# Performance work log

Hardware: AMD Instinct MI355X
Metric: run time of the kernel (lower is better)

## Reference

```python
import jax, jax.numpy as jnp
import numpy as np


def setup_inputs() -> dict:
    key = jax.random.key(0)
    k1, k2, k3 = jax.random.split(key, 3)
    B, H, N, D = 4, 16, 4096, 128
    return {
        "q": jax.random.normal(k1, (B, H, N, D), dtype=jnp.float32),
        "k": jax.random.normal(k2, (B, H, N, D), dtype=jnp.float32),
        "v": jax.random.normal(k3, (B, H, N, D), dtype=jnp.float32),
    }


def reference(q, k, v):
    # Aaren-style numerically stable online-softmax linear-attention scan.
    # q, k, v: [B, H, N, D]
    scale = 1.0
    B, H, N, D = q.shape
    qs = jnp.moveaxis(q * scale, 2, 0)  # [N, B, H, D] time-major
    ks = jnp.moveaxis(k, 2, 0)
    vs = jnp.moveaxis(v, 2, 0)

    n0 = jnp.zeros((B, H, D), dtype=q.dtype)
    d0 = jnp.zeros((B, H, 1), dtype=q.dtype)
    m0 = jnp.full((B, H, 1), -jnp.inf, dtype=q.dtype)

    def step(carry, inp):
        n_p, d_p, m_p = carry
        q_t, k_t, v_t = inp
        alpha = jnp.sum(q_t * k_t, axis=-1, keepdims=True)  # [B, H, 1]
        m_t = jnp.maximum(m_p, alpha)
        exp_mdiff = jnp.exp(m_p - m_t)
        exp_adiff = jnp.exp(alpha - m_t)
        d_t = exp_mdiff * d_p + exp_adiff
        n_t = exp_mdiff * n_p + exp_adiff * v_t
        y_t = n_t / d_t
        return (n_t, d_t, m_t), y_t

    _, y = jax.lax.scan(step, (n0, d0, m0), (qs, ks, vs))  # y: [N, B, H, D]
    return jnp.moveaxis(y, 0, 2)  # [B, H, N, D]
```

## Files before the change

kernel.cpp:

```cpp
#include <hip/hip_runtime.h>
#include <math.h>
#include <stdint.h>

static constexpr int ROWS = 64;
static constexpr int NSEQ = 4096;
static constexpr int DIM  = 128;
static constexpr int SC   = 16;
static constexpr int SPR  = NSEQ / SC;
static constexpr int NSC  = ROWS * SPR;
static constexpr int VC   = 64;
static constexpr int VPR  = NSEQ / VC;
static constexpr int NVC  = ROWS * VPR;
static constexpr int SPC  = VC / SC;

__global__ __launch_bounds__(256) void k_alpha(
    const float* __restrict__ q, const float* __restrict__ k,
    float* __restrict__ alpha, float* __restrict__ cM, float* __restrict__ cD)
{
    const int lane = threadIdx.x & 31;
    const int g    = blockIdx.x * 8 + (threadIdx.x >> 5);
    const int t    = lane >> 1;
    const int h    = lane & 1;
    const float* qb = q + (size_t)g * (SC * DIM) + t * DIM + h * 64;
    const float* kb = k + (size_t)g * (SC * DIM) + t * DIM + h * 64;

    float acc = 0.f;
    #pragma unroll
    for (int u0 = 0; u0 < 64; u0 += 16) {
        float4 q4[4], k4[4];
        #pragma unroll
        for (int j = 0; j < 4; ++j) q4[j] = *(const float4*)(qb + u0 + j * 4);
        #pragma unroll
        for (int j = 0; j < 4; ++j) k4[j] = *(const float4*)(kb + u0 + j * 4);
        __builtin_amdgcn_sched_barrier(0);
        #pragma unroll
        for (int j = 0; j < 4; ++j)
            acc += q4[j].x * k4[j].x + q4[j].y * k4[j].y
                 + q4[j].z * k4[j].z + q4[j].w * k4[j].w;
    }
    acc += __shfl_xor(acc, 1);

    float M = acc;
    M = fmaxf(M, __shfl_xor(M, 2));
    M = fmaxf(M, __shfl_xor(M, 4));
    M = fmaxf(M, __shfl_xor(M, 8));
    M = fmaxf(M, __shfl_xor(M, 16));
    float e = (h == 0) ? __expf(acc - M) : 0.f;
    e += __shfl_xor(e, 2);
    e += __shfl_xor(e, 4);
    e += __shfl_xor(e, 8);
    e += __shfl_xor(e, 16);

    if (h == 0) alpha[g * SC + t] = acc;
    if (lane == 0) { cM[g] = M; cD[g] = e; }
}

__global__ __launch_bounds__(256) void k_scan(
    const float* __restrict__ alpha, const float* __restrict__ cM,
    const float* __restrict__ cD,
    float* __restrict__ pM, float* __restrict__ pD, float2* __restrict__ coefCW)
{
    __shared__ float lM[SPR], lD[SPR], lpM[SPR];
    const int row = blockIdx.x;
    const int tid = threadIdx.x;

    lM[tid] = cM[row * SPR + tid];
    lD[tid] = cD[row * SPR + tid];
    __syncthreads();

    if (tid == 0) {
        float m = -INFINITY, d = 0.f;
        for (int sl = 0; sl < SPR; ++sl) {
            lpM[sl] = m;
            pM[row * SPR + sl] = m; pD[row * SPR + sl] = d;
            const float M = lM[sl], D = lD[sl];
            const float mn = fmaxf(m, M);
            d = d * __expf(m - mn) + D * __expf(M - mn);
            m = mn;
        }
    }
    __syncthreads();

    const int li = tid & 15, grp = tid >> 4;
    for (int sl = grp; sl < SPR; sl += 16) {
        const int s = row * SPR + sl;
        const float a = alpha[s * SC + li];
        float m = a;
        #pragma unroll
        for (int d = 1; d < 16; d <<= 1) {
            const float o = __shfl_up(m, d, 16);
            if (li >= d) m = fmaxf(m, o);
        }
        const float carry = lpM[sl];
        const float mf = fmaxf(m, carry);
        float mp = __shfl_up(mf, 1, 16);
        if (li == 0) mp = carry;
        const float cc = __expf(mp - mf);
        const float wt = __expf(a - mf);
        coefCW[s * SC + li] = make_float2(cc, wt);
    }
}

__global__ __launch_bounds__(256) void k_agg(
    const float* __restrict__ v, const float2* __restrict__ coefCW,
    float2* __restrict__ aggN)
{
    const int lane  = threadIdx.x & 63;
    const int C     = blockIdx.x * 4 + (threadIdx.x >> 6);
    const int vbase = C * (VC * DIM);
    const int cbase = __builtin_amdgcn_readfirstlane(C * VC);

    float nx = 0.f, ny = 0.f;
    for (int t0 = 0; t0 < VC; t0 += 8) {
        float2 cw[8], vv[8];
        #pragma unroll
        for (int u = 0; u < 8; ++u) cw[u] = coefCW[cbase + t0 + u];
        #pragma unroll
        for (int u = 0; u < 8; ++u)
            vv[u] = *((const float2*)(v + vbase + (t0 + u) * DIM) + lane);
        #pragma unroll
        for (int u = 0; u < 8; ++u) {
            nx = cw[u].x * nx + cw[u].y * vv[u].x;
            ny = cw[u].x * ny + cw[u].y * vv[u].y;
        }
    }
    aggN[C * (DIM / 2) + lane] = make_float2(nx, ny);
}

__global__ __launch_bounds__(128) void k_pref(
    float* __restrict__ aggN, const float* __restrict__ pM)
{
    const int row = blockIdx.x;
    const int d   = threadIdx.x;
    float state = 0.f;
    for (int C0 = 0; C0 < VPR; C0 += 8) {
        float nb[8], f1[8];
        #pragma unroll
        for (int u = 0; u < 8; ++u) {
            const int C  = C0 + u;
            const int Cg = row * VPR + C;
            nb[u] = aggN[Cg * DIM + d];
            const bool last = (C == VPR - 1);
            const float mp  = pM[SPC * Cg];
            const float mp2 = last ? 0.f : pM[SPC * Cg + SPC];
            f1[u] = last ? 0.f : __expf(mp - mp2);
        }
        #pragma unroll
        for (int u = 0; u < 8; ++u) {
            const float nc = nb[u];
            aggN[(row * VPR + C0 + u) * DIM + d] = state;
            state = state * f1[u] + nc;
        }
    }
}

__global__ __launch_bounds__(256) void k_out(
    const float* __restrict__ v, const float2* __restrict__ coefCW,
    const float2* __restrict__ preN, const float* __restrict__ pD,
    float* __restrict__ y)
{
    const int lane  = threadIdx.x & 63;
    const int C     = blockIdx.x * 4 + (threadIdx.x >> 6);
    const int vbase = C * (VC * DIM);
    const int cbase = __builtin_amdgcn_readfirstlane(C * VC);

    float2 n  = preN[C * (DIM / 2) + lane];
    float dch = pD[SPC * C];

    for (int t0 = 0; t0 < VC; t0 += 8) {
        float2 cw[8], vv[8];
        #pragma unroll
        for (int u = 0; u < 8; ++u) cw[u] = coefCW[cbase + t0 + u];
        #pragma unroll
        for (int u = 0; u < 8; ++u)
            vv[u] = *((const float2*)(v + vbase + (t0 + u) * DIM) + lane);
        #pragma unroll
        for (int u = 0; u < 8; ++u) {
            n.x = cw[u].x * n.x + cw[u].y * vv[u].x;
            n.y = cw[u].x * n.y + cw[u].y * vv[u].y;
            dch = cw[u].x * dch + cw[u].y;
            const float rd = __builtin_amdgcn_rcpf(dch);
            *((float2*)(y + vbase + (t0 + u) * DIM) + lane) =
                make_float2(n.x * rd, n.y * rd);
        }
    }
}

extern "C" void kernel_launch(void* const* d_in, const int* in_sizes, int n_in,
                              void* d_out, int out_size, void* d_ws, size_t ws_size,
                              hipStream_t stream) {
    const float* q = (const float*)d_in[0];
    const float* k = (const float*)d_in[1];
    const float* v = (const float*)d_in[2];
    float* y  = (float*)d_out;
    float* ws = (float*)d_ws;

    float*  coefCWf = ws;
    float*  pM      = coefCWf + 2 * ROWS * NSEQ;
    float*  pD      = pM + NSC;
    float*  cM      = pD + NSC;
    float*  cD      = cM + NSC;
    float*  U       = cD + NSC;
    float*  alphaA  = U;
    float*  aggNf   = U;
    float2* coefCW  = (float2*)coefCWf;
    float2* aggN2   = (float2*)aggNf;

    k_alpha<<<NSC / 8, 256, 0, stream>>>(q, k, alphaA, cM, cD);
    k_scan<<<ROWS, 256, 0, stream>>>(alphaA, cM, cD, pM, pD, coefCW);
    k_agg<<<NVC / 4, 256, 0, stream>>>(v, coefCW, aggN2);
    k_pref<<<ROWS, DIM, 0, stream>>>(aggNf, pM);
    k_out<<<NVC / 4, 256, 0, stream>>>(v, coefCW, aggN2, pD, y);
}
```

Measured before the change: 175.8 us.

## Stage q/k tiles into LDS via direct global-to-LDS loads in k_alpha

Rewrites the alpha kernel so each 256-thread block handles one 16-row chunk. It loads q and k straight into shared memory with global_load_lds using an XOR swizzle, then reads swizzled float4s to compute partial dot products and reduces them across waves through shared memory. The aim is fully coalesced, asynchronous loads and more blocks in flight in place of per-thread strided float4 loads. In exchange it adds two block barriers and much more LDS per block, and only 16 threads do the final reduction.

Result: faster. 159.6 us (-9.2%).

```diff
diff --git a/kernel.cpp b/kernel.cpp
--- a/kernel.cpp
+++ b/kernel.cpp
@@ -13,46 +13,69 @@
 static constexpr int NVC  = ROWS * VPR;
 static constexpr int SPC  = VC / SC;
 
+typedef __attribute__((address_space(3))) uint32_t  lds_u32;
+typedef const __attribute__((address_space(1))) uint32_t g_u32;
+
 __global__ __launch_bounds__(256) void k_alpha(
     const float* __restrict__ q, const float* __restrict__ k,
     float* __restrict__ alpha, float* __restrict__ cM, float* __restrict__ cD)
 {
-    const int lane = threadIdx.x & 31;
-    const int g    = blockIdx.x * 8 + (threadIdx.x >> 5);
-    const int t    = lane >> 1;
-    const int h    = lane & 1;
-    const float* qb = q + (size_t)g * (SC * DIM) + t * DIM + h * 64;
-    const float* kb = k + (size_t)g * (SC * DIM) + t * DIM + h * 64;
-
-    float acc = 0.f;
+    __shared__ float qs[2048];
+    __shared__ float ks[2048];
+    __shared__ float aw[4][16];
+    const int tid = threadIdx.x;
+    const int l   = tid & 63;
+    const int w   = tid >> 6;
+    const int s   = blockIdx.x;
+    const size_t base = (size_t)s * (SC * DIM);
+
     #pragma unroll
-    for (int u0 = 0; u0 < 64; u0 += 16) {
-        float4 q4[4], k4[4];
-        #pragma unroll
-        for (int j = 0; j < 4; ++j) q4[j] = *(const float4*)(qb + u0 + j * 4);
-        #pragma unroll
-        for (int j = 0; j < 4; ++j) k4[j] = *(const float4*)(kb + u0 + j * 4);
-        __builtin_amdgcn_sched_barrier(0);
-        #pragma unroll
-        for (int j = 0; j < 4; ++j)
-            acc += q4[j].x * k4[j].x + q4[j].y * k4[j].y
-                 + q4[j].z * k4[j].z + q4[j].w * k4[j].w;
-    }
-    acc += __shfl_xor(acc, 1);
-
-    float M = acc;
-    M = fmaxf(M, __shfl_xor(M, 2));
-    M = fmaxf(M, __shfl_xor(M, 4));
-    M = fmaxf(M, __shfl_xor(M, 8));
-    M = fmaxf(M, __shfl_xor(M, 16));
-    float e = (h == 0) ? __expf(acc - M) : 0.f;
-    e += __shfl_xor(e, 2);
-    e += __shfl_xor(e, 4);
-    e += __shfl_xor(e, 8);
-    e += __shfl_xor(e, 16);
-
-    if (h == 0) alpha[g * SC + t] = acc;
-    if (lane == 0) { cM[g] = M; cD[g] = e; }
+    for (int r = 0; r < 2; ++r) {
+        const int p  = r * 4096 + tid * 16;
+        const int ps = p ^ (((p >> 9) & 7) << 4);
+        __builtin_amdgcn_global_load_lds((g_u32*)(q + base + (ps >> 2)),
+            (lds_u32*)&qs[(r * 4096 + w * 1024) >> 2], 16, 0, 0);
+    }
+    #pragma unroll
+    for (int r = 0; r < 2; ++r) {
+        const int p  = r * 4096 + tid * 16;
+        const int ps = p ^ (((p >> 9) & 7) << 4);
+        __builtin_amdgcn_global_load_lds((g_u32*)(k + base + (ps >> 2)),
+            (lds_u32*)&ks[(r * 4096 + w * 1024) >> 2], 16, 0, 0);
+    }
+    __syncthreads();
+
+    const int row = l & 15;
+    const int cb  = (l >> 4) + 4 * w;
+    const int swz = (row & 7) << 4;
+    float part = 0.f;
+    #pragma unroll
+    for (int rr = 0; rr < 2; ++rr) {
+        const int off = row * 512 + ((cb * 32 + rr * 16) ^ swz);
+        const float4 qv = *(const float4*)((const char*)qs + off);
+        const float4 kv = *(const float4*)((const char*)ks + off);
+        part += qv.x * kv.x + qv.y * kv.y + qv.z * kv.z + qv.w * kv.w;
+    }
+    part += __shfl_xor(part, 16);
+    part += __shfl_xor(part, 32);
+    if (l < 16) aw[w][row] = part;
+    __syncthreads();
+
+    if (tid < 16) {
+        const float a = aw[0][tid] + aw[1][tid] + aw[2][tid] + aw[3][tid];
+        float M = a;
+        M = fmaxf(M, __shfl_xor(M, 1));
+        M = fmaxf(M, __shfl_xor(M, 2));
+        M = fmaxf(M, __shfl_xor(M, 4));
+        M = fmaxf(M, __shfl_xor(M, 8));
+        float e = __expf(a - M);
+        e += __shfl_xor(e, 1);
+        e += __shfl_xor(e, 2);
+        e += __shfl_xor(e, 4);
+        e += __shfl_xor(e, 8);
+        alpha[s * SC + tid] = a;
+        if (tid == 0) { cM[s] = M; cD[s] = e; }
+    }
 }
 
 __global__ __launch_bounds__(256) void k_scan(
@@ -206,7 +229,7 @@
     float2* coefCW  = (float2*)coefCWf;
     float2* aggN2   = (float2*)aggNf;
 
-    k_alpha<<<NSC / 8, 256, 0, stream>>>(q, k, alphaA, cM, cD);
+    k_alpha<<<NSC, 256, 0, stream>>>(q, k, alphaA, cM, cD);
     k_scan<<<ROWS, 256, 0, stream>>>(alphaA, cM, cD, pM, pD, coefCW);
     k_agg<<<NVC / 4, 256, 0, stream>>>(v, coefCW, aggN2);
     k_pref<<<ROWS, DIM, 0, stream>>>(aggNf, pM);
```

## Stream q/k through LDS with async double-buffered loads in k_alpha

Applied to the files above, without the earlier changes.

Rewrites the dot-product kernel so each wave owns 64 timesteps and stages q and k rows into LDS with global_load_lds. The loads are double-buffered, using vmcnt waits to overlap fetch with compute. The scan chunk size drops from 16 to 8, so chunk max/sum stats are formed from pairs of 4-row tiles, and k_scan is adapted to 8-wide segments. This targets better memory-level parallelism on the large q/k read, at the cost of doubling the serial single-thread carry scan in k_scan.

Measured after the change: 171.6 us. 2.4% less time.

```diff
diff --git a/kernel.cpp b/kernel.cpp
--- a/kernel.cpp
+++ b/kernel.cpp
@@ -5,7 +5,7 @@
 static constexpr int ROWS = 64;
 static constexpr int NSEQ = 4096;
 static constexpr int DIM  = 128;
-static constexpr int SC   = 16;
+static constexpr int SC   = 8;
 static constexpr int SPR  = NSEQ / SC;
 static constexpr int NSC  = ROWS * SPR;
 static constexpr int VC   = 64;
@@ -13,46 +13,85 @@
 static constexpr int NVC  = ROWS * VPR;
 static constexpr int SPC  = VC / SC;
 
+typedef __attribute__((address_space(3))) uint32_t  lds_u32;
+typedef const __attribute__((address_space(1))) uint32_t g_u32;
+
 __global__ __launch_bounds__(256) void k_alpha(
     const float* __restrict__ q, const float* __restrict__ k,
     float* __restrict__ alpha, float* __restrict__ cM, float* __restrict__ cD)
 {
-    const int lane = threadIdx.x & 31;
-    const int g    = blockIdx.x * 8 + (threadIdx.x >> 5);
-    const int t    = lane >> 1;
-    const int h    = lane & 1;
-    const float* qb = q + (size_t)g * (SC * DIM) + t * DIM + h * 64;
-    const float* kb = k + (size_t)g * (SC * DIM) + t * DIM + h * 64;
-
-    float acc = 0.f;
+    __shared__ float lds[4 * 2048];
+    const int tid  = threadIdx.x;
+    const int l    = tid & 63;
+    const int w    = tid >> 6;
+    const int x    = l & 15;
+    const int gr   = l >> 4;
+    const int wgid = blockIdx.x * 4 + w;
+    const float* qw = q + (size_t)wgid * (64 * DIM);
+    const float* kw = k + (size_t)wgid * (64 * DIM);
+    const int wl = w * 2048;
+
+    float aT[16], sM[8], sD[8];
+
+    #define STAGE(J)                                                          \
+        do {                                                                  \
+            const int _b = wl + ((J) & 1) * 1024;                             \
+            _Pragma("unroll")                                                 \
+            for (int r = 0; r < 2; ++r) {                                     \
+                __builtin_amdgcn_global_load_lds(                             \
+                    (g_u32*)(qw + (J) * 512 + r * 256 + l * 4),               \
+                    (lds_u32*)&lds[_b + r * 256], 16, 0, 0);                  \
+                __builtin_amdgcn_global_load_lds(                             \
+                    (g_u32*)(kw + (J) * 512 + r * 256 + l * 4),               \
+                    (lds_u32*)&lds[_b + 512 + r * 256], 16, 0, 0);            \
+            }                                                                 \
+        } while (0)
+
+    STAGE(0);
+    STAGE(1);
+
+    float aPrev = 0.f;
     #pragma unroll
-    for (int u0 = 0; u0 < 64; u0 += 16) {
-        float4 q4[4], k4[4];
-        #pragma unroll
-        for (int j = 0; j < 4; ++j) q4[j] = *(const float4*)(qb + u0 + j * 4);
-        #pragma unroll
-        for (int j = 0; j < 4; ++j) k4[j] = *(const float4*)(kb + u0 + j * 4);
+    for (int j = 0; j < 16; ++j) {
+        if (j < 15) asm volatile("s_waitcnt vmcnt(4)" ::: "memory");
+        else        asm volatile("s_waitcnt vmcnt(0)" ::: "memory");
+        const float* tb = &lds[wl + (j & 1) * 1024];
+        const float4 q0 = *(const float4*)(tb + gr * 128 + x * 8);
+        const float4 q1 = *(const float4*)(tb + gr * 128 + x * 8 + 4);
+        const float4 k0 = *(const float4*)(tb + 512 + gr * 128 + x * 8);
+        const float4 k1 = *(const float4*)(tb + 512 + gr * 128 + x * 8 + 4);
+        float p = q0.x*k0.x + q0.y*k0.y + q0.z*k0.z + q0.w*k0.w
+                + q1.x*k1.x + q1.y*k1.y + q1.z*k1.z + q1.w*k1.w;
+        p += __shfl_xor(p, 1);
+        p += __shfl_xor(p, 2);
+        p += __shfl_xor(p, 4);
+        p += __shfl_xor(p, 8);
+        aT[j] = p;
         __builtin_amdgcn_sched_barrier(0);
-        #pragma unroll
-        for (int j = 0; j < 4; ++j)
-            acc += q4[j].x * k4[j].x + q4[j].y * k4[j].y
-                 + q4[j].z * k4[j].z + q4[j].w * k4[j].w;
-    }
-    acc += __shfl_xor(acc, 1);
-
-    float M = acc;
-    M = fmaxf(M, __shfl_xor(M, 2));
-    M = fmaxf(M, __shfl_xor(M, 4));
-    M = fmaxf(M, __shfl_xor(M, 8));
-    M = fmaxf(M, __shfl_xor(M, 16));
-    float e = (h == 0) ? __expf(acc - M) : 0.f;
-    e += __shfl_xor(e, 2);
-    e += __shfl_xor(e, 4);
-    e += __shfl_xor(e, 8);
-    e += __shfl_xor(e, 16);
-
-    if (h == 0) alpha[g * SC + t] = acc;
-    if (lane == 0) { cM[g] = M; cD[g] = e; }
+        if (j < 14) STAGE(j + 2);
+        if (j & 1) {
+            float M = fmaxf(aPrev, p);
+            M = fmaxf(M, __shfl_xor(M, 16));
+            M = fmaxf(M, __shfl_xor(M, 32));
+            float e = __expf(aPrev - M) + __expf(p - M);
+            e += __shfl_xor(e, 16);
+            e += __shfl_xor(e, 32);
+            sM[j >> 1] = M; sD[j >> 1] = e;
+        }
+        aPrev = p;
+    }
+    #undef STAGE
+
+    #pragma unroll
+    for (int j = 0; j < 16; ++j)
+        if (x == 0) alpha[wgid * 64 + j * 4 + gr] = aT[j];
+    if (l == 0) {
+        #pragma unroll
+        for (int p2 = 0; p2 < 8; ++p2) {
+            cM[wgid * 8 + p2] = sM[p2];
+            cD[wgid * 8 + p2] = sD[p2];
+        }
+    }
 }
 
 __global__ __launch_bounds__(256) void k_scan(
@@ -64,8 +103,10 @@
     const int row = blockIdx.x;
     const int tid = threadIdx.x;
 
-    lM[tid] = cM[row * SPR + tid];
-    lD[tid] = cD[row * SPR + tid];
+    lM[tid]       = cM[row * SPR + tid];
+    lM[tid + 256] = cM[row * SPR + tid + 256];
+    lD[tid]       = cD[row * SPR + tid];
+    lD[tid + 256] = cD[row * SPR + tid + 256];
     __syncthreads();
 
     if (tid == 0) {
@@ -81,19 +122,19 @@
     }
     __syncthreads();
 
-    const int li = tid & 15, grp = tid >> 4;
-    for (int sl = grp; sl < SPR; sl += 16) {
+    const int li = tid & 7, grp = tid >> 3;
+    for (int sl = grp; sl < SPR; sl += 32) {
         const int s = row * SPR + sl;
         const float a = alpha[s * SC + li];
         float m = a;
         #pragma unroll
-        for (int d = 1; d < 16; d <<= 1) {
-            const float o = __shfl_up(m, d, 16);
+        for (int d = 1; d < 8; d <<= 1) {
+            const float o = __shfl_up(m, d, 8);
             if (li >= d) m = fmaxf(m, o);
         }
         const float carry = lpM[sl];
         const float mf = fmaxf(m, carry);
-        float mp = __shfl_up(mf, 1, 16);
+        float mp = __shfl_up(mf, 1, 8);
         if (li == 0) mp = carry;
         const float cc = __expf(mp - mf);
         const float wt = __expf(a - mf);
@@ -206,7 +247,7 @@
     float2* coefCW  = (float2*)coefCWf;
     float2* aggN2   = (float2*)aggNf;
 
-    k_alpha<<<NSC / 8, 256, 0, stream>>>(q, k, alphaA, cM, cD);
+    k_alpha<<<1024, 256, 0, stream>>>(q, k, alphaA, cM, cD);
     k_scan<<<ROWS, 256, 0, stream>>>(alphaA, cM, cD, pM, pD, coefCW);
     k_agg<<<NVC / 4, 256, 0, stream>>>(v, coefCW, aggN2);
     k_pref<<<ROWS, DIM, 0, stream>>>(aggNf, pM);
```
